# Kernel optimization log

Hardware: AMD Instinct MI355X
Metric: run time of the kernel (lower is better)

Reference implementation:

```python
import jax, jax.numpy as jnp
import numpy as np

B = 16384        # batch_size
D = 128          # d_model
V = 1_000_000    # vocab size
S = 5            # negative_sample_size


def setup_inputs() -> dict:
    key = jax.random.key(0)
    k1, k2, k3, k4 = jax.random.split(key, 4)
    h = jax.random.normal(k1, (B, D), dtype=jnp.float32)
    emb_table = jax.random.normal(k2, (V, D), dtype=jnp.float32)
    target_index = jax.random.randint(k3, (B,), 0, V, dtype=jnp.int64)
    neg_index = jax.random.randint(k4, (B, S), 0, V, dtype=jnp.int64)
    return {"h": h, "emb_table": emb_table, "target_index": target_index, "neg_index": neg_index}


def reference(h, emb_table, target_index, neg_index):
    # positive: gather (B,D), dot with h -> (B,1), sigmoid
    e_pos = emb_table[target_index]                      # (B, D)
    pos_out = jax.nn.sigmoid(jnp.sum(h * e_pos, axis=-1, keepdims=True))  # (B, 1)
    pos_label = jnp.ones((B, 1), dtype=h.dtype)
    # negative: gather (B,S,D), batched dot -> (B,S), sigmoid
    e_neg = emb_table[neg_index]                         # (B, S, D)
    neg_out = jax.nn.sigmoid(jnp.einsum('bd,bsd->bs', h, e_neg))          # (B, S)
    neg_label = jnp.zeros((B, S), dtype=h.dtype)
    return (pos_out, pos_label, neg_out, neg_label)
```

## Files before the change

kernel.cpp:

```cpp
#include <hip/hip_runtime.h>
#include <math.h>

#define NB 16384
#define ND 128
#define NS 5

__global__ __launch_bounds__(256) void ws_negsamp_kernel(
    const float* __restrict__ h,
    const float* __restrict__ emb,
    const int*   __restrict__ tgt,
    const int*   __restrict__ neg,
    float*       __restrict__ out)
{
    const int wave = (blockIdx.x * blockDim.x + threadIdx.x) >> 6;
    const int lane = threadIdx.x & 63;
    if (wave >= NB) return;
    const int row = wave;

    const float2 hv = *reinterpret_cast<const float2*>(h + (size_t)row * ND + lane * 2);

    int idx[6];
    idx[0] = tgt[row];
#pragma unroll
    for (int s = 0; s < NS; ++s) idx[s + 1] = neg[row * NS + s];

    float myres = 0.0f;
#pragma unroll
    for (int j = 0; j < 6; ++j) {
        const float2 ev =
            *reinterpret_cast<const float2*>(emb + (size_t)idx[j] * ND + lane * 2);
        float sum = hv.x * ev.x + hv.y * ev.y;
#pragma unroll
        for (int off = 32; off >= 1; off >>= 1)
            sum += __shfl_xor(sum, off, 64);
        const float sig = 1.0f / (1.0f + __expf(-sum));
        if (lane == j) myres = sig;
    }

    if (lane == 0) {
        out[row]      = myres;
        out[NB + row] = 1.0f;
    } else if (lane <= NS) {
        const int s = lane - 1;
        out[2 * NB + row * NS + s]           = myres;
        out[2 * NB + NB * NS + row * NS + s] = 0.0f;
    }
}

extern "C" void kernel_launch(void* const* d_in, const int* in_sizes, int n_in,
                              void* d_out, int out_size, void* d_ws, size_t ws_size,
                              hipStream_t stream) {
    const float* h   = (const float*)d_in[0];
    const float* emb = (const float*)d_in[1];
    const int*   tgt = (const int*)d_in[2];
    const int*   neg = (const int*)d_in[3];
    float*       out = (float*)d_out;

    const int blocks = NB / 4;
    ws_negsamp_kernel<<<blocks, 256, 0, stream>>>(h, emb, tgt, neg, out);
}
```

Before: 558.6 us.

## Process two rows per wavefront with float4 loads and batched shuffle reductions

Each 64-lane wave now handles two batch rows, one per 32-lane half, and loads h and embeddings as float4 instead of float2. All six embedding loads are issued before any arithmetic, and the six dot-product reductions are interleaved across a 5-step shuffle tree instead of six serial 6-step trees. The grid is halved and launch bounds ask for higher occupancy. The aim is more memory-level parallelism for the random gathers and less shuffle latency, at the cost of more registers per thread and serialized per-lane output stores.

```diff
diff --git a/kernel.cpp b/kernel.cpp
--- a/kernel.cpp
+++ b/kernel.cpp
@@ -5,7 +5,7 @@
 #define ND 128
 #define NS 5
 
-__global__ __launch_bounds__(256) void ws_negsamp_kernel(
+__global__ __launch_bounds__(256, 8) void ws_negsamp_kernel(
     const float* __restrict__ h,
     const float* __restrict__ emb,
     const int*   __restrict__ tgt,
@@ -14,36 +14,42 @@
 {
     const int wave = (blockIdx.x * blockDim.x + threadIdx.x) >> 6;
     const int lane = threadIdx.x & 63;
-    if (wave >= NB) return;
-    const int row = wave;
+    const int half = lane >> 5;
+    const int hl   = lane & 31;
+    const int row  = wave * 2 + half;
 
-    const float2 hv = *reinterpret_cast<const float2*>(h + (size_t)row * ND + lane * 2);
+    const float4 hv = *reinterpret_cast<const float4*>(h + (size_t)row * ND + hl * 4);
 
     int idx[6];
     idx[0] = tgt[row];
 #pragma unroll
     for (int s = 0; s < NS; ++s) idx[s + 1] = neg[row * NS + s];
 
-    float myres = 0.0f;
+    float4 ev[6];
 #pragma unroll
-    for (int j = 0; j < 6; ++j) {
-        const float2 ev =
-            *reinterpret_cast<const float2*>(emb + (size_t)idx[j] * ND + lane * 2);
-        float sum = hv.x * ev.x + hv.y * ev.y;
+    for (int j = 0; j < 6; ++j)
+        ev[j] = *reinterpret_cast<const float4*>(emb + (size_t)idx[j] * ND + hl * 4);
+
+    float sum[6];
 #pragma unroll
-        for (int off = 32; off >= 1; off >>= 1)
-            sum += __shfl_xor(sum, off, 64);
-        const float sig = 1.0f / (1.0f + __expf(-sum));
-        if (lane == j) myres = sig;
+    for (int j = 0; j < 6; ++j)
+        sum[j] = hv.x * ev[j].x + hv.y * ev[j].y + hv.z * ev[j].z + hv.w * ev[j].w;
+
+#pragma unroll
+    for (int off = 16; off >= 1; off >>= 1) {
+#pragma unroll
+        for (int j = 0; j < 6; ++j)
+            sum[j] += __shfl_xor(sum[j], off, 64);
     }
 
-    if (lane == 0) {
-        out[row]      = myres;
+    if (hl == 0) {
+        out[row]      = 1.0f / (1.0f + __expf(-sum[0]));
         out[NB + row] = 1.0f;
-    } else if (lane <= NS) {
-        const int s = lane - 1;
-        out[2 * NB + row * NS + s]           = myres;
-        out[2 * NB + NB * NS + row * NS + s] = 0.0f;
+#pragma unroll
+        for (int s = 0; s < NS; ++s) {
+            out[2 * NB + row * NS + s]           = 1.0f / (1.0f + __expf(-sum[s + 1]));
+            out[2 * NB + NB * NS + row * NS + s] = 0.0f;
+        }
     }
 }
 
@@ -56,6 +62,6 @@
     const int*   neg = (const int*)d_in[3];
     float*       out = (float*)d_out;
 
-    const int blocks = NB / 4;
+    const int blocks = NB / 8;
     ws_negsamp_kernel<<<blocks, 256, 0, stream>>>(h, emb, tgt, neg, out);
 }
```

Result: no change. 559.7 us (+0.2%).
